# Performance work log

Hardware: AMD Instinct MI355X
Metric: run time of the kernel (lower is better)

Reference implementation:

```python
import jax, jax.numpy as jnp
import numpy as np

K = 3            # num_neighbors
C_IN = 128       # in_channels (== out_channels, required by fusion_kernel)
C_OUT = 128
B, H, W = 2, 64, 512
EPS = 1e-5       # BatchNorm eps (eval mode, running stats)


def _unfold(x, k):
    # F.unfold(x, k, padding=k//2).view(B, C, k*k, H*W); patch index = kh*k + kw
    b, c, h, w = x.shape
    p = k // 2
    xp = jnp.pad(x, ((0, 0), (0, 0), (p, p), (p, p)))
    patches = jnp.stack(
        [xp[:, :, i:i + h, j:j + w] for i in range(k) for j in range(k)], axis=2
    )  # (B, C, k*k, H, W)
    return patches.reshape(b, c, k * k, h * w)


def _conv1x1(x, w):
    # 1x1 Conv2d (bias=False) on (B, C, K^2, HW)
    return jnp.einsum('oc,bcnp->bonp', w, x)


def _bn(x, g, b, m, v):
    # BatchNorm2d in eval mode with running stats
    scale = (g / jnp.sqrt(v + EPS))[None, :, None, None]
    shift = (b - m * g / jnp.sqrt(v + EPS))[None, :, None, None]
    return x * scale + shift


def setup_inputs() -> dict:
    key = jax.random.key(0)
    ks = jax.random.split(key, 9)
    f32 = jnp.float32
    features = jax.random.normal(ks[0], (B, C_IN, H, W), f32)
    cart = jax.random.normal(ks[1], (B, 3, H, W), f32)
    mask = jax.random.bernoulli(ks[2], 0.9, (B, 1, H, W))

    def bn_params(k, c):
        k1, k2, k3, k4 = jax.random.split(k, 4)
        g = 1.0 + 0.1 * jax.random.normal(k1, (c,), f32)
        b = 0.1 * jax.random.normal(k2, (c,), f32)
        m = 0.1 * jax.random.normal(k3, (c,), f32)
        v = jax.random.uniform(k4, (c,), f32, 0.5, 1.5)
        return g, b, m, v

    pw = jax.random.normal(ks[3], (C_OUT, 3), f32) / jnp.sqrt(3.0)
    pg, pb, pm, pv = bn_params(ks[4], C_OUT)
    fw = jax.random.normal(ks[5], (C_OUT, C_IN), f32) / jnp.sqrt(float(C_IN))
    fg, fb, fm, fv = bn_params(ks[6], C_OUT)
    ew = jax.random.normal(ks[7], (3, C_OUT), f32) / jnp.sqrt(float(C_OUT))
    eg, eb, em, ev = bn_params(ks[8], 3)
    return dict(features=features, cart=cart, mask=mask,
                pw=pw, pg=pg, pb=pb, pm=pm, pv=pv,
                fw=fw, fg=fg, fb=fb, fm=fm, fv=fv,
                ew=ew, eg=eg, eb=eb, em=em, ev=ev)


def reference(features, cart, mask, pw, pg, pb, pm, pv,
              fw, fg, fb, fm, fv, ew, eg, eb, em, ev):
    b, c, h, w = features.shape
    fdt = features.dtype
    fe = _unfold(features, K)                      # (B, C, K^2, HW)
    cc = _unfold(cart, K)                          # (B, 3, K^2, HW)
    mu = _unfold(mask.astype(fdt), K)              # (B, 1, K^2, HW)
    center = (K * K) // 2
    rel = cc - cc[:, :, center:center + 1]         # relative coordinates
    pos = jax.nn.relu(_bn(_conv1x1(rel, pw), pg, pb, pm, pv))
    fe = jax.nn.relu(_bn(_conv1x1(fe, fw), fg, fb, fm, fv)) + pos
    geo = jnp.max(fe * mu, axis=2, keepdims=True)  # max_pool over K^2 neighbors
    e2c = _bn(_conv1x1(geo, ew), eg, eb, em, ev).reshape(b, 3, h, w)
    cart_out = cart + e2c * mask.astype(cart.dtype)
    return geo.reshape(b, -1, h, w), cart_out
```

## Files before the change

kernel.cpp:

```cpp
#include <hip/hip_runtime.h>

typedef unsigned short u16;
typedef unsigned int u32;
typedef unsigned char u8;

#define HW 32768
#define NPX 65536
#define GEO_SIZE 8388608
#define EPS 1e-5f

#define OFF_PWP   0
#define OFF_EWP   512
#define OFF_SHE   1024
#define OFF_FLG   1028
#define OFF_SHF   1088
#define W2T_OFF   8192
#define EAP_OFF   131072
#define T_OFF     8388608

#define LDS_STRIDE 136

typedef __bf16 bf16x8 __attribute__((ext_vector_type(8)));
typedef float f32x4 __attribute__((ext_vector_type(4)));
typedef float f32x2 __attribute__((ext_vector_type(2)));

__device__ __forceinline__ float bf2f(u16 u){ return __uint_as_float(((u32)u) << 16); }
__device__ __forceinline__ u16 f2bf(float f){
  u32 x = __float_as_uint(f);
  return (u16)((x + 0x7fffu + ((x >> 16) & 1u)) >> 16);
}
__device__ __forceinline__ float bflo(u32 w){ return __uint_as_float(w << 16); }
__device__ __forceinline__ float bfhi(u32 w){ return __uint_as_float(w & 0xffff0000u); }

__device__ __forceinline__ f32x2 pk_fma(f32x2 a, f32x2 b, f32x2 c){
  return __builtin_elementwise_fma(a, b, c);
}
__device__ __forceinline__ f32x2 pk_max(f32x2 a, f32x2 b){
  return __builtin_elementwise_max(a, b);
}

__device__ __forceinline__ float ldp(const void* p, int i, bool isbf){
  return isbf ? bf2f(((const u16*)p)[i]) : ((const float*)p)[i];
}

__device__ __forceinline__ bool sniff_bf16(const void* fv){
  const u16* w = (const u16*)fv;
  int hits = 0;
  for (int i = 0; i < 32; i++) {
    float v = bf2f(w[i]);
    hits += (v >= 0.45f && v <= 1.55f) ? 1 : 0;
  }
  return hits >= 26;
}

__device__ __forceinline__ int sniff_mask(const void* mask){
  const u8* mb = (const u8*)mask;
  int c01 = 0, ones = 0;
  for (int i = 0; i < 64; i++) { u8 v = mb[i]; c01 += (v <= 1); ones += (v == 1); }
  if (c01 == 64) return (ones >= 24) ? 0 : 1;
  const u16* mw = (const u16*)mask;
  int c3f = 0;
  for (int i = 0; i < 32; i++) c3f += (mw[i] == 0x3F80);
  return (c3f >= 22) ? 2 : 3;
}

__device__ __forceinline__ float mask_at(const void* m, int gi, int enc){
  if (enc == 0) return ((const u8*)m)[gi]  ? 1.f : 0.f;
  if (enc == 1) return ((const int*)m)[gi] ? 1.f : 0.f;
  if (enc == 2) return ((const u16*)m)[gi] ? 1.f : 0.f;
  return (((const float*)m)[gi] != 0.f) ? 1.f : 0.f;
}

__global__ __launch_bounds__(256) void prep_kernel(
    const void* __restrict__ pw, const void* __restrict__ pg,
    const void* __restrict__ pb, const void* __restrict__ pm,
    const void* __restrict__ pv,
    const void* __restrict__ fw, const void* __restrict__ fg,
    const void* __restrict__ fb, const void* __restrict__ fm,
    const void* __restrict__ fv,
    const void* __restrict__ ew, const void* __restrict__ eg,
    const void* __restrict__ eb, const void* __restrict__ em,
    const void* __restrict__ ev,
    const void* __restrict__ mask,
    float* __restrict__ ws){
  int blk = blockIdx.x, tid = threadIdx.x;
  bool isbf = sniff_bf16(fv);
  if (blk < 32) {
    int p = blk * 256 + tid;
    int o = p >> 6;
    float sf = ldp(fg, o, isbf) * __frsqrt_rn(ldp(fv, o, isbf) + EPS);
    u32 outv;
    if (isbf) {
      u32 in = ((const u32*)fw)[p];
      outv = (u32)f2bf(sf * bf2f((u16)(in & 0xffff))) |
             ((u32)f2bf(sf * bf2f((u16)(in >> 16))) << 16);
    } else {
      const float* fwp = (const float*)fw;
      outv = (u32)f2bf(sf * fwp[2 * p]) | ((u32)f2bf(sf * fwp[2 * p + 1]) << 16);
    }
    ((u32*)((char*)ws + W2T_OFF))[p] = outv;
    return;
  }
  int o = tid;
  if (o == 0) {
    ws[OFF_FLG]     = isbf ? 1.f : 0.f;
    ws[OFF_FLG + 1] = (float)sniff_mask(mask);
  }
  if (o < 128) {
    float sf = ldp(fg, o, isbf) * __frsqrt_rn(ldp(fv, o, isbf) + EPS);
    ws[OFF_SHF + o] = ldp(fb, o, isbf) - ldp(fm, o, isbf) * sf;
    float sp = ldp(pg, o, isbf) * __frsqrt_rn(ldp(pv, o, isbf) + EPS);
    float4* pwp = (float4*)(ws + OFF_PWP);
    pwp[o] = make_float4(sp * ldp(pw, o * 3 + 0, isbf),
                         sp * ldp(pw, o * 3 + 1, isbf),
                         sp * ldp(pw, o * 3 + 2, isbf),
                         ldp(pb, o, isbf) - ldp(pm, o, isbf) * sp);
    float se0 = ldp(eg, 0, isbf) * __frsqrt_rn(ldp(ev, 0, isbf) + EPS);
    float se1 = ldp(eg, 1, isbf) * __frsqrt_rn(ldp(ev, 1, isbf) + EPS);
    float se2 = ldp(eg, 2, isbf) * __frsqrt_rn(ldp(ev, 2, isbf) + EPS);
    float4* ewp = (float4*)(ws + OFF_EWP);
    ewp[o] = make_float4(se0 * ldp(ew, 0 * 128 + o, isbf),
                         se1 * ldp(ew, 1 * 128 + o, isbf),
                         se2 * ldp(ew, 2 * 128 + o, isbf), 0.f);
    if (o < 3) {
      float se = ldp(eg, o, isbf) * __frsqrt_rn(ldp(ev, o, isbf) + EPS);
      ws[OFF_SHE + o] = ldp(eb, o, isbf) - ldp(em, o, isbf) * se;
    }
  }
}

__global__ __launch_bounds__(256) void stage1_kernel(const void* __restrict__ feat,
                                                     const float* __restrict__ ws,
                                                     u16* __restrict__ t){
  __shared__ u16 lds[128 * LDS_STRIDE];
  int tid = threadIdx.x;
  bool isbf = ws[OFF_FLG] > 0.5f;
  int pxg = blockIdx.x * 128;
  int b = pxg >> 15, hw0 = pxg & 32767;

  {
    int cp = tid & 63, q = tid >> 6;
    int c0 = cp * 2;
    long e0 = (long)(b * 128 + c0) * HW + hw0 + q * 32;
    u16* base = lds + (q * 32) * LDS_STRIDE + c0;
    if (isbf) {
      const uint4* g0 = (const uint4*)((const u16*)feat + e0);
      const uint4* g1 = (const uint4*)((const u16*)feat + e0 + HW);
#pragma unroll
      for (int i = 0; i < 4; i++) {
        uint4 a = g0[i], c = g1[i];
        u32 av[4] = {a.x, a.y, a.z, a.w};
        u32 cv[4] = {c.x, c.y, c.z, c.w};
#pragma unroll
        for (int k = 0; k < 4; k++) {
          u32 lo = (av[k] & 0xffffu) | (cv[k] << 16);
          u32 hi = (av[k] >> 16) | (cv[k] & 0xffff0000u);
          *(u32*)(base + (i * 8 + k * 2 + 0) * LDS_STRIDE) = lo;
          *(u32*)(base + (i * 8 + k * 2 + 1) * LDS_STRIDE) = hi;
        }
      }
    } else {
      const float4* g0 = (const float4*)((const float*)feat + e0);
      const float4* g1 = (const float4*)((const float*)feat + e0 + HW);
#pragma unroll
      for (int i = 0; i < 8; i++) {
        float4 a = g0[i], c = g1[i];
        float av[4] = {a.x, a.y, a.z, a.w};
        float cv[4] = {c.x, c.y, c.z, c.w};
#pragma unroll
        for (int k = 0; k < 4; k++) {
          u32 v = (u32)f2bf(av[k]) | ((u32)f2bf(cv[k]) << 16);
          *(u32*)(base + (i * 4 + k) * LDS_STRIDE) = v;
        }
      }
    }
  }
  __syncthreads();

  int wave = tid >> 6, lane = tid & 63;
  int ln = lane & 15, quad = lane >> 4;
  int pxw = wave * 32;
  const uint4* W = (const uint4*)((const char*)ws + W2T_OFF);

  f32x4 acc[8][2];
#pragma unroll
  for (int ot = 0; ot < 8; ot++)
#pragma unroll
    for (int pt = 0; pt < 2; pt++) acc[ot][pt] = (f32x4){0.f, 0.f, 0.f, 0.f};

#pragma unroll
  for (int ks = 0; ks < 4; ks++) {
    bf16x8 a[8], bfr[2];
#pragma unroll
    for (int ot = 0; ot < 8; ot++)
      a[ot] = __builtin_bit_cast(bf16x8, W[(ot * 16 + ln) * 16 + ks * 4 + quad]);
#pragma unroll
    for (int pt = 0; pt < 2; pt++)
      bfr[pt] = __builtin_bit_cast(bf16x8,
          *(const uint4*)(lds + (pxw + pt * 16 + ln) * LDS_STRIDE + ks * 32 + quad * 8));
#pragma unroll
    for (int ot = 0; ot < 8; ot++)
#pragma unroll
      for (int pt = 0; pt < 2; pt++)
        acc[ot][pt] = __builtin_amdgcn_mfma_f32_16x16x32_bf16(a[ot], bfr[pt], acc[ot][pt], 0, 0, 0);
  }
  __syncthreads();

  const float* shf = ws + OFF_SHF;
#pragma unroll
  for (int ot = 0; ot < 8; ot++) {
#pragma unroll
    for (int r = 0; r < 4; r++) {
      int o = ot * 16 + quad * 4 + r;
      float s = shf[o];
#pragma unroll
      for (int pt = 0; pt < 2; pt++) {
        float v = fmaxf(acc[ot][pt][r] + s, 0.f);
        lds[o * LDS_STRIDE + pxw + pt * 16 + ln] = f2bf(v);
      }
    }
  }
  __syncthreads();
  {
    int o = tid >> 1, half = tid & 1;
    const u16* src = lds + o * LDS_STRIDE + half * 64;
    uint4* dst = (uint4*)(t + o * NPX + pxg + half * 64);
#pragma unroll
    for (int k = 0; k < 8; k++) dst[k] = *(const uint4*)(src + k * 8);
  }
}

__global__ __launch_bounds__(256) void stage2_kernel(const void* __restrict__ cart,
                                                     const float* __restrict__ ws,
                                                     const void* __restrict__ rawmask,
                                                     const u16* __restrict__ t,
                                                     float* __restrict__ eap,
                                                     void* __restrict__ out){
  int tid = threadIdx.x;
  int pxb = blockIdx.x & 127, grp = blockIdx.x >> 7;
  int px0 = pxb * 512 + tid * 2;
  int b = px0 >> 15, hw = px0 & 32767;
  int h = hw >> 9, w = hw & 511;
  bool isbf = ws[OFF_FLG] > 0.5f;
  int enc = (int)ws[OFF_FLG + 1];

  f32x2 rel2[9][3];
  f32x2 mv2[9];
  {
    float cr[12][3];
    float mm[12];
#pragma unroll
    for (int r = 0; r < 3; r++) {
#pragma unroll
      for (int c = 0; c < 4; c++) {
        int idx = r * 4 + c;
        int h2 = h + r - 1, w2 = w + c - 1;
        bool ok = ((unsigned)h2 < 64u) && ((unsigned)w2 < 512u);
        int hw2 = ok ? ((h2 << 9) | w2) : hw;
        int gi = b * HW + hw2;
        mm[idx] = ok ? mask_at(rawmask, gi, enc) : 0.f;
#pragma unroll
        for (int d = 0; d < 3; d++)
          cr[idx][d] = isbf ? bf2f(((const u16*)cart)[(b * 3 + d) * HW + hw2])
                            : ((const float*)cart)[(b * 3 + d) * HW + hw2];
      }
    }
#pragma unroll
    for (int r = 0; r < 3; r++)
#pragma unroll
      for (int cc = 0; cc < 3; cc++) {
        int n = r * 3 + cc;
        mv2[n] = (f32x2){mm[r * 4 + cc], mm[r * 4 + cc + 1]};
#pragma unroll
        for (int d = 0; d < 3; d++)
          rel2[n][d] = (f32x2){cr[r * 4 + cc][d] - cr[5][d],
                               cr[r * 4 + cc + 1][d] - cr[6][d]};
      }
  }

  const float4* pwp = (const float4*)(ws + OFF_PWP);
  const float4* ewp = (const float4*)(ws + OFF_EWP);
  f32x2 eA = {0.f, 0.f}, eB = {0.f, 0.f}, eC = {0.f, 0.f};
  u16* o16 = (u16*)out;
  float* of = (float*)out;
  const f32x2 zero2 = {0.f, 0.f};

#pragma unroll 4
  for (int j = 0; j < 32; j++) {
    int o = grp * 32 + j;
    const u16* tb = t + o * NPX + b * HW;
    u32 tw[3][3];
#pragma unroll
    for (int r = 0; r < 3; r++) {
      const u32* rp = (const u32*)(tb + (h + r - 1) * 512 + (w - 2));
      tw[r][0] = rp[0]; tw[r][1] = rp[1]; tw[r][2] = rp[2];
    }
    float4 P = pwp[o];
    f32x2 Px = {P.x, P.x}, Py = {P.y, P.y}, Pz = {P.z, P.z}, Pw = {P.w, P.w};
    f32x2 g = {0.f, 0.f};
#pragma unroll
    for (int r = 0; r < 3; r++) {
      float tm1 = bfhi(tw[r][0]);
      float t0  = bflo(tw[r][1]);
      float tp1 = bfhi(tw[r][1]);
      float tp2 = bflo(tw[r][2]);
      f32x2 tv[3] = {{tm1, t0}, {t0, tp1}, {tp1, tp2}};
#pragma unroll
      for (int cc = 0; cc < 3; cc++) {
        int n = r * 3 + cc;
        f32x2 pos = pk_max(pk_fma(Px, rel2[n][0],
                           pk_fma(Py, rel2[n][1],
                           pk_fma(Pz, rel2[n][2], Pw))), zero2);
        g = pk_max(g, (tv[cc] + pos) * mv2[n]);
      }
    }
    int gi = (b * 128 + o) * HW + hw;
    if (isbf) *(u32*)(o16 + gi) = (u32)f2bf(g.x) | ((u32)f2bf(g.y) << 16);
    else { of[gi] = g.x; of[gi + 1] = g.y; }
    float4 E = ewp[o];
    eA = pk_fma((f32x2){E.x, E.x}, g, eA);
    eB = pk_fma((f32x2){E.y, E.y}, g, eB);
    eC = pk_fma((f32x2){E.z, E.z}, g, eC);
  }
  *(f32x2*)(eap + (grp * 3 + 0) * NPX + px0) = eA;
  *(f32x2*)(eap + (grp * 3 + 1) * NPX + px0) = eB;
  *(f32x2*)(eap + (grp * 3 + 2) * NPX + px0) = eC;
}

__global__ __launch_bounds__(256) void final_kernel(const void* __restrict__ cart,
                                                    const float* __restrict__ ws,
                                                    const void* __restrict__ rawmask,
                                                    const float* __restrict__ eap,
                                                    void* __restrict__ out){
  int px0 = (blockIdx.x * 256 + threadIdx.x) * 2;
  int b = px0 >> 15, hw = px0 & 32767;
  bool isbf = ws[OFF_FLG] > 0.5f;
  int enc = (int)ws[OFF_FLG + 1];
  f32x2 s0 = {0.f, 0.f}, s1 = {0.f, 0.f}, s2 = {0.f, 0.f};
#pragma unroll
  for (int g = 0; g < 4; g++) {
    s0 += *(const f32x2*)(eap + (g * 3 + 0) * NPX + px0);
    s1 += *(const f32x2*)(eap + (g * 3 + 1) * NPX + px0);
    s2 += *(const f32x2*)(eap + (g * 3 + 2) * NPX + px0);
  }
  float m0 = mask_at(rawmask, b * HW + hw, enc);
  float m1 = mask_at(rawmask, b * HW + hw + 1, enc);
  float she0 = ws[OFF_SHE], she1 = ws[OFF_SHE + 1], she2 = ws[OFF_SHE + 2];
  float c0a, c0b, c1a, c1b, c2a, c2b;
  if (isbf) {
    const u16* cb = (const u16*)cart + b * 3 * HW;
    c0a = bf2f(cb[hw]); c0b = bf2f(cb[hw + 1]);
    c1a = bf2f(cb[HW + hw]); c1b = bf2f(cb[HW + hw + 1]);
    c2a = bf2f(cb[2 * HW + hw]); c2b = bf2f(cb[2 * HW + hw + 1]);
  } else {
    const float* cb = (const float*)cart + b * 3 * HW;
    c0a = cb[hw]; c0b = cb[hw + 1];
    c1a = cb[HW + hw]; c1b = cb[HW + hw + 1];
    c2a = cb[2 * HW + hw]; c2b = cb[2 * HW + hw + 1];
  }
  float r0a = c0a + (s0.x + she0) * m0, r0b = c0b + (s0.y + she0) * m1;
  float r1a = c1a + (s1.x + she1) * m0, r1b = c1b + (s1.y + she1) * m1;
  float r2a = c2a + (s2.x + she2) * m0, r2b = c2b + (s2.y + she2) * m1;
  int cbase = GEO_SIZE + b * 3 * HW + hw;
  if (isbf) {
    u16* o16 = (u16*)out;
    *(u32*)(o16 + cbase)          = (u32)f2bf(r0a) | ((u32)f2bf(r0b) << 16);
    *(u32*)(o16 + cbase + HW)     = (u32)f2bf(r1a) | ((u32)f2bf(r1b) << 16);
    *(u32*)(o16 + cbase + 2 * HW) = (u32)f2bf(r2a) | ((u32)f2bf(r2b) << 16);
  } else {
    float* of = (float*)out;
    of[cbase] = r0a; of[cbase + 1] = r0b;
    of[cbase + HW] = r1a; of[cbase + HW + 1] = r1b;
    of[cbase + 2 * HW] = r2a; of[cbase + 2 * HW + 1] = r2b;
  }
}

extern "C" void kernel_launch(void* const* d_in, const int* in_sizes, int n_in,
                              void* d_out, int out_size, void* d_ws, size_t ws_size,
                              hipStream_t stream) {
  const void* feat = d_in[0];
  const void* cart = d_in[1];
  const void* mask = d_in[2];
  float* ws  = (float*)d_ws;
  float* eap = (float*)((char*)d_ws + EAP_OFF);
  u16*  t    = (u16*)((char*)d_ws + T_OFF);

  hipLaunchKernelGGL(prep_kernel, dim3(33), dim3(256), 0, stream,
                     d_in[3], d_in[4], d_in[5], d_in[6], d_in[7],
                     d_in[8], d_in[9], d_in[10], d_in[11], d_in[12],
                     d_in[13], d_in[14], d_in[15], d_in[16], d_in[17],
                     mask, ws);
  hipLaunchKernelGGL(stage1_kernel, dim3(512), dim3(256), 0, stream, feat, ws, t);
  hipLaunchKernelGGL(stage2_kernel, dim3(512), dim3(256), 0, stream, cart, ws, mask, t, eap, d_out);
  hipLaunchKernelGGL(final_kernel, dim3(128), dim3(256), 0, stream, cart, ws, mask, eap, d_out);
}
```

Measured before the change: 164.9 us.

## Fold prep and final kernels into stage1/stage2 with last-block atomic reduction

Removes the separate parameter-prep kernel by having stage1 read raw fw directly (applying BN scale in the epilogue) and stage2 compute its pos/edge BN-folded weights into shared memory. The final reduction kernel is eliminated by a per-pixel-block atomic counter: the last of the four channel-group blocks sums partial edge contributions and writes cart_out. This cuts two launches and their serialization gaps. In exchange every block redundantly recomputes parameters and sniffs the dtype and mask encoding, stage1 converts fp32 weights per block, and the result relies on atomic/fence ordering plus a counter reset done inside stage1.

```diff
diff --git a/kernel.cpp b/kernel.cpp
--- a/kernel.cpp
+++ b/kernel.cpp
@@ -9,14 +9,9 @@
 #define GEO_SIZE 8388608
 #define EPS 1e-5f
 
-#define OFF_PWP   0
-#define OFF_EWP   512
-#define OFF_SHE   1024
-#define OFF_FLG   1028
-#define OFF_SHF   1088
-#define W2T_OFF   8192
-#define EAP_OFF   131072
-#define T_OFF     8388608
+#define CNT_OFF  0
+#define EAP_OFF  4096
+#define T_OFF    8388608
 
 #define LDS_STRIDE 136
 
@@ -71,70 +66,24 @@
   return (((const float*)m)[gi] != 0.f) ? 1.f : 0.f;
 }
 
-__global__ __launch_bounds__(256) void prep_kernel(
-    const void* __restrict__ pw, const void* __restrict__ pg,
-    const void* __restrict__ pb, const void* __restrict__ pm,
-    const void* __restrict__ pv,
-    const void* __restrict__ fw, const void* __restrict__ fg,
-    const void* __restrict__ fb, const void* __restrict__ fm,
-    const void* __restrict__ fv,
-    const void* __restrict__ ew, const void* __restrict__ eg,
-    const void* __restrict__ eb, const void* __restrict__ em,
-    const void* __restrict__ ev,
-    const void* __restrict__ mask,
-    float* __restrict__ ws){
-  int blk = blockIdx.x, tid = threadIdx.x;
+__global__ __launch_bounds__(256) void stage1_kernel(const void* __restrict__ feat,
+                                                     const void* __restrict__ fw,
+                                                     const void* __restrict__ fg,
+                                                     const void* __restrict__ fb,
+                                                     const void* __restrict__ fm,
+                                                     const void* __restrict__ fv,
+                                                     char* __restrict__ wsb){
+  __shared__ u16 lds[128 * LDS_STRIDE];
+  __shared__ float sfa[128], sha[128];
+  u16* t = (u16*)(wsb + T_OFF);
+  int tid = threadIdx.x;
   bool isbf = sniff_bf16(fv);
-  if (blk < 32) {
-    int p = blk * 256 + tid;
-    int o = p >> 6;
-    float sf = ldp(fg, o, isbf) * __frsqrt_rn(ldp(fv, o, isbf) + EPS);
-    u32 outv;
-    if (isbf) {
-      u32 in = ((const u32*)fw)[p];
-      outv = (u32)f2bf(sf * bf2f((u16)(in & 0xffff))) |
-             ((u32)f2bf(sf * bf2f((u16)(in >> 16))) << 16);
-    } else {
-      const float* fwp = (const float*)fw;
-      outv = (u32)f2bf(sf * fwp[2 * p]) | ((u32)f2bf(sf * fwp[2 * p + 1]) << 16);
-    }
-    ((u32*)((char*)ws + W2T_OFF))[p] = outv;
-    return;
-  }
-  int o = tid;
-  if (o == 0) {
-    ws[OFF_FLG]     = isbf ? 1.f : 0.f;
-    ws[OFF_FLG + 1] = (float)sniff_mask(mask);
-  }
-  if (o < 128) {
-    float sf = ldp(fg, o, isbf) * __frsqrt_rn(ldp(fv, o, isbf) + EPS);
-    ws[OFF_SHF + o] = ldp(fb, o, isbf) - ldp(fm, o, isbf) * sf;
-    float sp = ldp(pg, o, isbf) * __frsqrt_rn(ldp(pv, o, isbf) + EPS);
-    float4* pwp = (float4*)(ws + OFF_PWP);
-    pwp[o] = make_float4(sp * ldp(pw, o * 3 + 0, isbf),
-                         sp * ldp(pw, o * 3 + 1, isbf),
-                         sp * ldp(pw, o * 3 + 2, isbf),
-                         ldp(pb, o, isbf) - ldp(pm, o, isbf) * sp);
-    float se0 = ldp(eg, 0, isbf) * __frsqrt_rn(ldp(ev, 0, isbf) + EPS);
-    float se1 = ldp(eg, 1, isbf) * __frsqrt_rn(ldp(ev, 1, isbf) + EPS);
-    float se2 = ldp(eg, 2, isbf) * __frsqrt_rn(ldp(ev, 2, isbf) + EPS);
-    float4* ewp = (float4*)(ws + OFF_EWP);
-    ewp[o] = make_float4(se0 * ldp(ew, 0 * 128 + o, isbf),
-                         se1 * ldp(ew, 1 * 128 + o, isbf),
-                         se2 * ldp(ew, 2 * 128 + o, isbf), 0.f);
-    if (o < 3) {
-      float se = ldp(eg, o, isbf) * __frsqrt_rn(ldp(ev, o, isbf) + EPS);
-      ws[OFF_SHE + o] = ldp(eb, o, isbf) - ldp(em, o, isbf) * se;
-    }
-  }
-}
-
-__global__ __launch_bounds__(256) void stage1_kernel(const void* __restrict__ feat,
-                                                     const float* __restrict__ ws,
-                                                     u16* __restrict__ t){
-  __shared__ u16 lds[128 * LDS_STRIDE];
-  int tid = threadIdx.x;
-  bool isbf = ws[OFF_FLG] > 0.5f;
+  if (blockIdx.x == 0 && tid < 128) ((u32*)(wsb + CNT_OFF))[tid] = 0;
+  if (tid < 128) {
+    float sf = ldp(fg, tid, isbf) * __frsqrt_rn(ldp(fv, tid, isbf) + EPS);
+    sfa[tid] = sf;
+    sha[tid] = ldp(fb, tid, isbf) - ldp(fm, tid, isbf) * sf;
+  }
   int pxg = blockIdx.x * 128;
   int b = pxg >> 15, hw0 = pxg & 32767;
 
@@ -180,7 +129,6 @@
   int wave = tid >> 6, lane = tid & 63;
   int ln = lane & 15, quad = lane >> 4;
   int pxw = wave * 32;
-  const uint4* W = (const uint4*)((const char*)ws + W2T_OFF);
 
   f32x4 acc[8][2];
 #pragma unroll
@@ -191,9 +139,25 @@
 #pragma unroll
   for (int ks = 0; ks < 4; ks++) {
     bf16x8 a[8], bfr[2];
-#pragma unroll
-    for (int ot = 0; ot < 8; ot++)
-      a[ot] = __builtin_bit_cast(bf16x8, W[(ot * 16 + ln) * 16 + ks * 4 + quad]);
+    if (isbf) {
+      const uint4* Wq = (const uint4*)fw;
+#pragma unroll
+      for (int ot = 0; ot < 8; ot++)
+        a[ot] = __builtin_bit_cast(bf16x8, Wq[(ot * 16 + ln) * 16 + ks * 4 + quad]);
+    } else {
+      const float* Wf = (const float*)fw;
+#pragma unroll
+      for (int ot = 0; ot < 8; ot++) {
+        int base = (ot * 16 + ln) * 128 + ks * 32 + quad * 8;
+        float4 lo = *(const float4*)(Wf + base);
+        float4 hi = *(const float4*)(Wf + base + 4);
+        uint4 p = make_uint4((u32)f2bf(lo.x) | ((u32)f2bf(lo.y) << 16),
+                             (u32)f2bf(lo.z) | ((u32)f2bf(lo.w) << 16),
+                             (u32)f2bf(hi.x) | ((u32)f2bf(hi.y) << 16),
+                             (u32)f2bf(hi.z) | ((u32)f2bf(hi.w) << 16));
+        a[ot] = __builtin_bit_cast(bf16x8, p);
+      }
+    }
 #pragma unroll
     for (int pt = 0; pt < 2; pt++)
       bfr[pt] = __builtin_bit_cast(bf16x8,
@@ -206,16 +170,15 @@
   }
   __syncthreads();
 
-  const float* shf = ws + OFF_SHF;
 #pragma unroll
   for (int ot = 0; ot < 8; ot++) {
 #pragma unroll
     for (int r = 0; r < 4; r++) {
       int o = ot * 16 + quad * 4 + r;
-      float s = shf[o];
+      float sf = sfa[o], sh = sha[o];
 #pragma unroll
       for (int pt = 0; pt < 2; pt++) {
-        float v = fmaxf(acc[ot][pt][r] + s, 0.f);
+        float v = fmaxf(fmaf(acc[ot][pt][r], sf, sh), 0.f);
         lds[o * LDS_STRIDE + pxw + pt * 16 + ln] = f2bf(v);
       }
     }
@@ -231,18 +194,55 @@
 }
 
 __global__ __launch_bounds__(256) void stage2_kernel(const void* __restrict__ cart,
-                                                     const float* __restrict__ ws,
                                                      const void* __restrict__ rawmask,
-                                                     const u16* __restrict__ t,
-                                                     float* __restrict__ eap,
+                                                     const void* __restrict__ pw,
+                                                     const void* __restrict__ pg,
+                                                     const void* __restrict__ pb,
+                                                     const void* __restrict__ pm,
+                                                     const void* __restrict__ pv,
+                                                     const void* __restrict__ ew,
+                                                     const void* __restrict__ eg,
+                                                     const void* __restrict__ eb,
+                                                     const void* __restrict__ em,
+                                                     const void* __restrict__ ev,
+                                                     const void* __restrict__ fv,
+                                                     char* __restrict__ wsb,
                                                      void* __restrict__ out){
+  __shared__ float sP[32][4];
+  __shared__ float sE[32][3];
+  __shared__ float sShe[3];
+  __shared__ int s_last;
+  u32* cnt = (u32*)(wsb + CNT_OFF);
+  float* eap = (float*)(wsb + EAP_OFF);
+  const u16* t = (const u16*)(wsb + T_OFF);
+
   int tid = threadIdx.x;
   int pxb = blockIdx.x & 127, grp = blockIdx.x >> 7;
+  bool isbf = sniff_bf16(fv);
+  int enc = sniff_mask(rawmask);
+
+  if (tid < 32) {
+    int o = grp * 32 + tid;
+    float sp = ldp(pg, o, isbf) * __frsqrt_rn(ldp(pv, o, isbf) + EPS);
+    sP[tid][0] = sp * ldp(pw, o * 3 + 0, isbf);
+    sP[tid][1] = sp * ldp(pw, o * 3 + 1, isbf);
+    sP[tid][2] = sp * ldp(pw, o * 3 + 2, isbf);
+    sP[tid][3] = ldp(pb, o, isbf) - ldp(pm, o, isbf) * sp;
+#pragma unroll
+    for (int d = 0; d < 3; d++) {
+      float se = ldp(eg, d, isbf) * __frsqrt_rn(ldp(ev, d, isbf) + EPS);
+      sE[tid][d] = se * ldp(ew, d * 128 + o, isbf);
+    }
+  }
+  if (tid < 3) {
+    float se = ldp(eg, tid, isbf) * __frsqrt_rn(ldp(ev, tid, isbf) + EPS);
+    sShe[tid] = ldp(eb, tid, isbf) - ldp(em, tid, isbf) * se;
+  }
+  __syncthreads();
+
   int px0 = pxb * 512 + tid * 2;
   int b = px0 >> 15, hw = px0 & 32767;
   int h = hw >> 9, w = hw & 511;
-  bool isbf = ws[OFF_FLG] > 0.5f;
-  int enc = (int)ws[OFF_FLG + 1];
 
   f32x2 rel2[9][3];
   f32x2 mv2[9];
@@ -278,8 +278,6 @@
       }
   }
 
-  const float4* pwp = (const float4*)(ws + OFF_PWP);
-  const float4* ewp = (const float4*)(ws + OFF_EWP);
   f32x2 eA = {0.f, 0.f}, eB = {0.f, 0.f}, eC = {0.f, 0.f};
   u16* o16 = (u16*)out;
   float* of = (float*)out;
@@ -295,8 +293,8 @@
       const u32* rp = (const u32*)(tb + (h + r - 1) * 512 + (w - 2));
       tw[r][0] = rp[0]; tw[r][1] = rp[1]; tw[r][2] = rp[2];
     }
-    float4 P = pwp[o];
-    f32x2 Px = {P.x, P.x}, Py = {P.y, P.y}, Pz = {P.z, P.z}, Pw = {P.w, P.w};
+    float Pxs = sP[j][0], Pys = sP[j][1], Pzs = sP[j][2], Pws = sP[j][3];
+    f32x2 Px = {Pxs, Pxs}, Py = {Pys, Pys}, Pz = {Pzs, Pzs}, Pw = {Pws, Pws};
     f32x2 g = {0.f, 0.f};
 #pragma unroll
     for (int r = 0; r < 3; r++) {
@@ -317,61 +315,60 @@
     int gi = (b * 128 + o) * HW + hw;
     if (isbf) *(u32*)(o16 + gi) = (u32)f2bf(g.x) | ((u32)f2bf(g.y) << 16);
     else { of[gi] = g.x; of[gi + 1] = g.y; }
-    float4 E = ewp[o];
-    eA = pk_fma((f32x2){E.x, E.x}, g, eA);
-    eB = pk_fma((f32x2){E.y, E.y}, g, eB);
-    eC = pk_fma((f32x2){E.z, E.z}, g, eC);
+    f32x2 Ex = {sE[j][0], sE[j][0]}, Ey = {sE[j][1], sE[j][1]}, Ez = {sE[j][2], sE[j][2]};
+    eA = pk_fma(Ex, g, eA);
+    eB = pk_fma(Ey, g, eB);
+    eC = pk_fma(Ez, g, eC);
   }
   *(f32x2*)(eap + (grp * 3 + 0) * NPX + px0) = eA;
   *(f32x2*)(eap + (grp * 3 + 1) * NPX + px0) = eB;
   *(f32x2*)(eap + (grp * 3 + 2) * NPX + px0) = eC;
-}
-
-__global__ __launch_bounds__(256) void final_kernel(const void* __restrict__ cart,
-                                                    const float* __restrict__ ws,
-                                                    const void* __restrict__ rawmask,
-                                                    const float* __restrict__ eap,
-                                                    void* __restrict__ out){
-  int px0 = (blockIdx.x * 256 + threadIdx.x) * 2;
-  int b = px0 >> 15, hw = px0 & 32767;
-  bool isbf = ws[OFF_FLG] > 0.5f;
-  int enc = (int)ws[OFF_FLG + 1];
-  f32x2 s0 = {0.f, 0.f}, s1 = {0.f, 0.f}, s2 = {0.f, 0.f};
-#pragma unroll
-  for (int g = 0; g < 4; g++) {
-    s0 += *(const f32x2*)(eap + (g * 3 + 0) * NPX + px0);
-    s1 += *(const f32x2*)(eap + (g * 3 + 1) * NPX + px0);
-    s2 += *(const f32x2*)(eap + (g * 3 + 2) * NPX + px0);
-  }
-  float m0 = mask_at(rawmask, b * HW + hw, enc);
-  float m1 = mask_at(rawmask, b * HW + hw + 1, enc);
-  float she0 = ws[OFF_SHE], she1 = ws[OFF_SHE + 1], she2 = ws[OFF_SHE + 2];
-  float c0a, c0b, c1a, c1b, c2a, c2b;
-  if (isbf) {
-    const u16* cb = (const u16*)cart + b * 3 * HW;
-    c0a = bf2f(cb[hw]); c0b = bf2f(cb[hw + 1]);
-    c1a = bf2f(cb[HW + hw]); c1b = bf2f(cb[HW + hw + 1]);
-    c2a = bf2f(cb[2 * HW + hw]); c2b = bf2f(cb[2 * HW + hw + 1]);
-  } else {
-    const float* cb = (const float*)cart + b * 3 * HW;
-    c0a = cb[hw]; c0b = cb[hw + 1];
-    c1a = cb[HW + hw]; c1b = cb[HW + hw + 1];
-    c2a = cb[2 * HW + hw]; c2b = cb[2 * HW + hw + 1];
-  }
-  float r0a = c0a + (s0.x + she0) * m0, r0b = c0b + (s0.y + she0) * m1;
-  float r1a = c1a + (s1.x + she1) * m0, r1b = c1b + (s1.y + she1) * m1;
-  float r2a = c2a + (s2.x + she2) * m0, r2b = c2b + (s2.y + she2) * m1;
-  int cbase = GEO_SIZE + b * 3 * HW + hw;
-  if (isbf) {
-    u16* o16 = (u16*)out;
-    *(u32*)(o16 + cbase)          = (u32)f2bf(r0a) | ((u32)f2bf(r0b) << 16);
-    *(u32*)(o16 + cbase + HW)     = (u32)f2bf(r1a) | ((u32)f2bf(r1b) << 16);
-    *(u32*)(o16 + cbase + 2 * HW) = (u32)f2bf(r2a) | ((u32)f2bf(r2b) << 16);
-  } else {
-    float* of = (float*)out;
-    of[cbase] = r0a; of[cbase + 1] = r0b;
-    of[cbase + HW] = r1a; of[cbase + HW + 1] = r1b;
-    of[cbase + 2 * HW] = r2a; of[cbase + 2 * HW + 1] = r2b;
+
+  __syncthreads();
+  if (tid == 0) {
+    __threadfence();
+    u32 old = __hip_atomic_fetch_add(&cnt[pxb], 1u, __ATOMIC_ACQ_REL,
+                                     __HIP_MEMORY_SCOPE_AGENT);
+    s_last = (old == 3u) ? 1 : 0;
+  }
+  __syncthreads();
+  if (s_last) {
+    __threadfence();
+    f32x2 s0 = {0.f, 0.f}, s1 = {0.f, 0.f}, s2 = {0.f, 0.f};
+#pragma unroll
+    for (int g = 0; g < 4; g++) {
+      s0 += *(const f32x2*)(eap + (g * 3 + 0) * NPX + px0);
+      s1 += *(const f32x2*)(eap + (g * 3 + 1) * NPX + px0);
+      s2 += *(const f32x2*)(eap + (g * 3 + 2) * NPX + px0);
+    }
+    float m0 = mask_at(rawmask, b * HW + hw, enc);
+    float m1 = mask_at(rawmask, b * HW + hw + 1, enc);
+    float she0 = sShe[0], she1 = sShe[1], she2 = sShe[2];
+    float c0a, c0b, c1a, c1b, c2a, c2b;
+    if (isbf) {
+      const u16* cb = (const u16*)cart + b * 3 * HW;
+      c0a = bf2f(cb[hw]); c0b = bf2f(cb[hw + 1]);
+      c1a = bf2f(cb[HW + hw]); c1b = bf2f(cb[HW + hw + 1]);
+      c2a = bf2f(cb[2 * HW + hw]); c2b = bf2f(cb[2 * HW + hw + 1]);
+    } else {
+      const float* cb = (const float*)cart + b * 3 * HW;
+      c0a = cb[hw]; c0b = cb[hw + 1];
+      c1a = cb[HW + hw]; c1b = cb[HW + hw + 1];
+      c2a = cb[2 * HW + hw]; c2b = cb[2 * HW + hw + 1];
+    }
+    float r0a = c0a + (s0.x + she0) * m0, r0b = c0b + (s0.y + she0) * m1;
+    float r1a = c1a + (s1.x + she1) * m0, r1b = c1b + (s1.y + she1) * m1;
+    float r2a = c2a + (s2.x + she2) * m0, r2b = c2b + (s2.y + she2) * m1;
+    int cbase = GEO_SIZE + b * 3 * HW + hw;
+    if (isbf) {
+      *(u32*)(o16 + cbase)          = (u32)f2bf(r0a) | ((u32)f2bf(r0b) << 16);
+      *(u32*)(o16 + cbase + HW)     = (u32)f2bf(r1a) | ((u32)f2bf(r1b) << 16);
+      *(u32*)(o16 + cbase + 2 * HW) = (u32)f2bf(r2a) | ((u32)f2bf(r2b) << 16);
+    } else {
+      of[cbase] = r0a; of[cbase + 1] = r0b;
+      of[cbase + HW] = r1a; of[cbase + HW + 1] = r1b;
+      of[cbase + 2 * HW] = r2a; of[cbase + 2 * HW + 1] = r2b;
+    }
   }
 }
 
@@ -381,16 +378,13 @@
   const void* feat = d_in[0];
   const void* cart = d_in[1];
   const void* mask = d_in[2];
-  float* ws  = (float*)d_ws;
-  float* eap = (float*)((char*)d_ws + EAP_OFF);
-  u16*  t    = (u16*)((char*)d_ws + T_OFF);
-
-  hipLaunchKernelGGL(prep_kernel, dim3(33), dim3(256), 0, stream,
+  char* wsb = (char*)d_ws;
+
+  hipLaunchKernelGGL(stage1_kernel, dim3(512), dim3(256), 0, stream,
+                     feat, d_in[8], d_in[9], d_in[10], d_in[11], d_in[12], wsb);
+  hipLaunchKernelGGL(stage2_kernel, dim3(512), dim3(256), 0, stream,
+                     cart, mask,
                      d_in[3], d_in[4], d_in[5], d_in[6], d_in[7],
-                     d_in[8], d_in[9], d_in[10], d_in[11], d_in[12],
                      d_in[13], d_in[14], d_in[15], d_in[16], d_in[17],
-                     mask, ws);
-  hipLaunchKernelGGL(stage1_kernel, dim3(512), dim3(256), 0, stream, feat, ws, t);
-  hipLaunchKernelGGL(stage2_kernel, dim3(512), dim3(256), 0, stream, cart, ws, mask, t, eap, d_out);
-  hipLaunchKernelGGL(final_kernel, dim3(128), dim3(256), 0, stream, cart, ws, mask, eap, d_out);
-}
+                     d_in[12], wsb, d_out);
+}
```

After: 199.9 us. 21.2% more time.
